# Kernel tuning notes

Measured on AMD Instinct MI355X. Metric: run time of the kernel, lower is better.

The kernel has to match this reference:

```python
import jax, jax.numpy as jnp
import numpy as np

EPS = 1e-7  # K.epsilon()
ROUTINGS = 3
NUM_CAPSULE = 32
DIM_CAPSULE = 16


def squash(x, axis=-1):
    s = jnp.sum(jnp.square(x), axis=axis, keepdims=True) + EPS
    scale = jnp.sqrt(s) / (0.5 + s)
    return scale * x


def setup_inputs() -> dict:
    key = jax.random.key(0)
    k1, k2 = jax.random.split(key)
    inputs = jax.random.normal(k1, (128, 1024, 128), dtype=jnp.float32)
    kernel = jax.random.normal(k2, (1, 128, NUM_CAPSULE * DIM_CAPSULE), dtype=jnp.float32) * 0.05
    return {"inputs": inputs, "kernel": kernel}


def reference(inputs, kernel):
    B, In, D = inputs.shape
    # shared-weight conv1d with kernel size 1 == GEMM over last dim
    hat = jnp.einsum('bid,dk->bik', inputs, kernel[0])  # (B, In, N*dc)
    hat = hat.reshape(B, In, NUM_CAPSULE, DIM_CAPSULE).transpose(0, 2, 1, 3)  # (B, N, In, dc)
    b = jnp.zeros((B, NUM_CAPSULE, In), dtype=hat.dtype)
    o = None
    for i in range(ROUTINGS):
        c = jax.nn.softmax(b, axis=1)                     # softmax over num_capsule
        o = squash(jnp.einsum('bni,bnid->bnd', c, hat))   # (B, N, dc)
        if i < ROUTINGS - 1:
            b = jnp.einsum('bnd,bnid->bni', o, hat)       # b = <o, hat> (replace, per code)
    return o
```

## Files before the change

### kernel.cpp

```cpp
#include <hip/hip_runtime.h>

#define BATCH 128
#define SEQ   1024
#define DIM   128
#define NCAP  32
#define DCAPS 16
#define KTOT  512
#define EPS_  1e-7f
#define RCH   8
#define RROWS 128

#define OFF_SPART 0
#define OFF_WT    (OFF_SPART + BATCH*RCH*DIM)
#define OFF_UBF   (OFF_WT + KTOT*DIM)
#define OFF_VP    (OFF_UBF + BATCH*NCAP*DIM/2)
#define OFF_XROW  (OFF_VP + BATCH*RCH*NCAP*DIM)
#define OFF_XT    (OFF_XROW + BATCH*SEQ*DIM/2)

typedef __attribute__((ext_vector_type(8))) short short8v;
typedef __attribute__((ext_vector_type(4))) float f32x4;
typedef unsigned short ushort_t;

__device__ __forceinline__ unsigned f2bf(float f) {
  unsigned u = __float_as_uint(f);
  u += 0x7fffu + ((u >> 16) & 1u);
  return u >> 16;
}
__device__ __forceinline__ uint4 pack8(float4 a, float4 b) {
  uint4 r;
  r.x = f2bf(a.x) | (f2bf(a.y) << 16);
  r.y = f2bf(a.z) | (f2bf(a.w) << 16);
  r.z = f2bf(b.x) | (f2bf(b.y) << 16);
  r.w = f2bf(b.z) | (f2bf(b.w) << 16);
  return r;
}

__global__ __launch_bounds__(256)
void k_pre(const float* __restrict__ x, const float* __restrict__ w,
           float* __restrict__ ws) {
  int t = threadIdx.x;
  __shared__ __align__(16) char smem[40960];

  if (blockIdx.y == BATCH) {
    float* wl = (float*)smem;
    int k0 = blockIdx.x * 64;
    for (int it = 0; it < 32; ++it) {
      int f = it * 256 + t;
      int kk = f & 63, d = f >> 6;
      wl[d * 66 + kk] = w[d * KTOT + k0 + kk];
    }
    __syncthreads();
    float* wt = ws + OFF_WT;
    for (int it = 0; it < 32; ++it) {
      int f = it * 256 + t;
      int d = f & 127, kk = f >> 7;
      wt[(size_t)(k0 + kk) * DIM + d] = wl[d * 66 + kk];
    }
    return;
  }
  int b = blockIdx.y, ch = blockIdx.x;
  ushort_t* xl = (ushort_t*)smem;
  float4* red0 = (float4*)(smem + 32768);
  float4* red1 = (float4*)(smem + 32768 + 4096);

  const float4* X4 = (const float4*)(x + ((size_t)b * SEQ + (size_t)ch * RROWS) * DIM);
  ushort_t* xrow = (ushort_t*)(ws + OFF_XROW) + ((size_t)b * SEQ + (size_t)ch * RROWS) * DIM;
  ushort_t* xt   = (ushort_t*)(ws + OFF_XT)   + (size_t)b * DIM * SEQ;

  int seg = t & 15, grp = t >> 4;
  float4 a0 = make_float4(0.f,0.f,0.f,0.f), a1 = make_float4(0.f,0.f,0.f,0.f);
  for (int it = 0; it < 8; ++it) {
    int r = it * 16 + grp;
    float4 v0 = X4[(size_t)r * 32 + seg * 2];
    float4 v1 = X4[(size_t)r * 32 + seg * 2 + 1];
    a0.x += v0.x; a0.y += v0.y; a0.z += v0.z; a0.w += v0.w;
    a1.x += v1.x; a1.y += v1.y; a1.z += v1.z; a1.w += v1.w;
    uint4 pk = pack8(v0, v1);
    *(uint4*)(xrow + (size_t)r * DIM + seg * 8) = pk;
    *(uint4*)(smem + r * 256 + ((seg << 4) ^ (((r >> 3) & 7) << 4))) = pk;
  }
  red0[grp * 16 + seg] = a0;
  red1[grp * 16 + seg] = a1;
  __syncthreads();

  if (t < 128) {
    int sg = t >> 3, e = t & 7;
    float s = 0.f;
    for (int g = 0; g < 16; ++g) {
      const float* p0 = (const float*)&red0[g * 16 + sg];
      const float* p1 = (const float*)&red1[g * 16 + sg];
      s += (e < 4) ? p0[e] : p1[e - 4];
    }
    ws[OFF_SPART + ((size_t)b * RCH + ch) * DIM + t] = s;
  }

  for (int j = 0; j < 8; ++j) {
    int f = j * 256 + t;
    int r8g = f & 15;
    int d   = f >> 4;
    int dhi = (d >> 3) << 4, dlo = (d & 7) * 2;
    int rsw = (r8g & 7) << 4;
    const char* base = smem + ((dhi ^ rsw) + dlo);
    union { ushort_t s[8]; uint4 v; } tmp;
    #pragma unroll
    for (int i = 0; i < 8; ++i)
      tmp.s[i] = *(const ushort_t*)(base + (r8g * 8 + i) * 256);
    *(uint4*)(xt + (size_t)d * SEQ + ch * RROWS + r8g * 8) = tmp.v;
  }
}

template<int MODE>
__global__ __launch_bounds__(128)
void k_ou(float* __restrict__ ws, float* __restrict__ outp) {
  int b = blockIdx.y, bx = blockIdx.x, t = threadIdx.x;
  int k = bx * 128 + t;
  __shared__ float vin[8 * DIM];
  __shared__ float osh[128];

  if (MODE == 0) {
    const float* sp = ws + OFF_SPART + (size_t)b * RCH * DIM;
    float s = 0.f;
    for (int c = 0; c < RCH; ++c) s += sp[c * DIM + t];
    vin[t] = s * (1.0f / 32.0f);
  } else {
    const float* vp = ws + OFF_VP + (size_t)b * RCH * NCAP * DIM + (size_t)bx * 8 * DIM;
    for (int j = 0; j < 8; ++j) {
      float s = 0.f;
      for (int c = 0; c < RCH; ++c)
        s += vp[(size_t)c * NCAP * DIM + j * DIM + t];
      vin[j * DIM + t] = s;
    }
  }
  __syncthreads();

  int nl = t >> 4;
  const float4* vr = (const float4*)((MODE == 0) ? vin : (vin + nl * DIM));
  const float4* wtr = (const float4*)(ws + OFF_WT + (size_t)k * DIM);
  float p = 0.f;
  #pragma unroll 8
  for (int i = 0; i < 32; ++i) {
    float4 wv = wtr[i], vv = vr[i];
    p += wv.x * vv.x + wv.y * vv.y + wv.z * vv.z + wv.w * vv.w;
  }

  float sq = p * p;
  sq += __shfl_xor(sq, 1, 16);
  sq += __shfl_xor(sq, 2, 16);
  sq += __shfl_xor(sq, 4, 16);
  sq += __shfl_xor(sq, 8, 16);
  sq += EPS_;
  float scale = sqrtf(sq) / (0.5f + sq);
  float o = scale * p;

  if (MODE == 2) { outp[(size_t)b * KTOT + k] = o; return; }

  osh[t] = o;
  __syncthreads();

  const float* wt = ws + OFF_WT;
  ushort_t* ubf = (ushort_t*)(ws + OFF_UBF) + (size_t)b * NCAP * DIM;
  for (int j = 0; j < 8; ++j) {
    int n = bx * 8 + j;
    float a = 0.f;
    #pragma unroll
    for (int dc = 0; dc < DCAPS; ++dc)
      a += wt[(size_t)(n * DCAPS + dc) * DIM + t] * osh[j * DCAPS + dc];
    ubf[(size_t)n * DIM + t] = (ushort_t)f2bf(a);
  }
}

__global__ __launch_bounds__(256)
void k_route(const float* __restrict__ ws_c, float* __restrict__ vp) {
  __shared__ __align__(16) ushort_t ct_s[NCAP * RROWS];

  int b = blockIdx.y, ch = blockIdx.x, t = threadIdx.x;
  int wv = t >> 6;
  int l  = t & 63;
  int q  = l >> 4;
  int lr = l & 15;

  const ushort_t* ubf  = (const ushort_t*)(ws_c + OFF_UBF) + (size_t)b * NCAP * DIM;
  const ushort_t* xrow = (const ushort_t*)(ws_c + OFF_XROW) + ((size_t)b * SEQ + (size_t)ch * RROWS) * DIM;
  const ushort_t* xt   = (const ushort_t*)(ws_c + OFF_XT)   + (size_t)b * DIM * SEQ + (size_t)ch * RROWS;

  short8v ufr[2][4], xfr[2][4];
  #pragma unroll
  for (int nt = 0; nt < 2; ++nt)
    #pragma unroll
    for (int kk = 0; kk < 4; ++kk)
      ufr[nt][kk] = *(const short8v*)(ubf + (size_t)(nt * 16 + lr) * DIM + kk * 32 + q * 8);
  #pragma unroll
  for (int rt = 0; rt < 2; ++rt)
    #pragma unroll
    for (int kk = 0; kk < 4; ++kk)
      xfr[rt][kk] = *(const short8v*)(xrow + (size_t)(wv * 32 + rt * 16 + lr) * DIM + kk * 32 + q * 8);

  f32x4 acc[2][2];
  #pragma unroll
  for (int rt = 0; rt < 2; ++rt)
    #pragma unroll
    for (int nt = 0; nt < 2; ++nt)
      acc[rt][nt] = (f32x4){0.f, 0.f, 0.f, 0.f};

  #pragma unroll
  for (int kk = 0; kk < 4; ++kk)
    #pragma unroll
    for (int rt = 0; rt < 2; ++rt)
      #pragma unroll
      for (int nt = 0; nt < 2; ++nt)
        acc[rt][nt] = __builtin_amdgcn_mfma_f32_16x16x32_bf16(
            ufr[nt][kk], xfr[rt][kk], acc[rt][nt], 0, 0, 0);

  short8v axfr[2][4];
  #pragma unroll
  for (int dt = 0; dt < 2; ++dt)
    #pragma unroll
    for (int kk = 0; kk < 4; ++kk)
      axfr[dt][kk] = *(const short8v*)(xt + (size_t)(wv * 32 + dt * 16 + lr) * SEQ + kk * 32 + q * 8);

  #pragma unroll
  for (int rt = 0; rt < 2; ++rt) {
    float v[8];
    #pragma unroll
    for (int nt = 0; nt < 2; ++nt)
      #pragma unroll
      for (int j = 0; j < 4; ++j) v[nt * 4 + j] = acc[rt][nt][j];
    float m = v[0];
    #pragma unroll
    for (int i = 1; i < 8; ++i) m = fmaxf(m, v[i]);
    m = fmaxf(m, __shfl_xor(m, 16));
    m = fmaxf(m, __shfl_xor(m, 32));
    float e[8], s = 0.f;
    #pragma unroll
    for (int i = 0; i < 8; ++i) { e[i] = __expf(v[i] - m); s += e[i]; }
    s += __shfl_xor(s, 16);
    s += __shfl_xor(s, 32);
    float inv = 1.0f / s;
    int r = wv * 32 + rt * 16 + lr;
    int rs = r >> 3, rb = (r & 7) * 2;
    #pragma unroll
    for (int nt = 0; nt < 2; ++nt)
      #pragma unroll
      for (int j = 0; j < 4; ++j) {
        int n = nt * 16 + q * 4 + j;
        *(ushort_t*)((char*)ct_s + n * 256 + ((rs ^ (n & 15)) << 4) + rb) =
            (ushort_t)f2bf(e[nt * 4 + j] * inv);
      }
  }

  __syncthreads();

  short8v bc[2][4];
  #pragma unroll
  for (int nt = 0; nt < 2; ++nt) {
    int n2 = nt * 16 + lr;
    #pragma unroll
    for (int kk = 0; kk < 4; ++kk)
      bc[nt][kk] = *(const short8v*)((char*)ct_s + n2 * 256 + (((4 * kk + q) ^ (n2 & 15)) << 4));
  }

  f32x4 vac[2][2];
  #pragma unroll
  for (int dt = 0; dt < 2; ++dt)
    #pragma unroll
    for (int nt = 0; nt < 2; ++nt)
      vac[dt][nt] = (f32x4){0.f, 0.f, 0.f, 0.f};

  #pragma unroll
  for (int kk = 0; kk < 4; ++kk)
    #pragma unroll
    for (int dt = 0; dt < 2; ++dt)
      #pragma unroll
      for (int nt = 0; nt < 2; ++nt)
        vac[dt][nt] = __builtin_amdgcn_mfma_f32_16x16x32_bf16(
            axfr[dt][kk], bc[nt][kk], vac[dt][nt], 0, 0, 0);

  float* vo = vp + ((size_t)(b * RCH + ch) * NCAP) * DIM;
  #pragma unroll
  for (int dt = 0; dt < 2; ++dt)
    #pragma unroll
    for (int nt = 0; nt < 2; ++nt) {
      int n = nt * 16 + lr;
      int d0 = wv * 32 + dt * 16 + q * 4;
      *(f32x4*)(vo + (size_t)n * DIM + d0) = vac[dt][nt];
    }
}

extern "C" void kernel_launch(void* const* d_in, const int* in_sizes, int n_in,
                              void* d_out, int out_size, void* d_ws, size_t ws_size,
                              hipStream_t stream) {
  (void)in_sizes; (void)n_in; (void)out_size; (void)ws_size;
  const float* x = (const float*)d_in[0];
  const float* w = (const float*)d_in[1];
  float* out = (float*)d_out;
  float* ws  = (float*)d_ws;
  float* wsvp = ws + OFF_VP;

  k_pre<<<dim3(8, BATCH + 1), 256, 0, stream>>>(x, w, ws);
  k_ou<0><<<dim3(4, BATCH), 128, 0, stream>>>(ws, out);
  k_route<<<dim3(RCH, BATCH), 256, 0, stream>>>(ws, wsvp);
  k_ou<1><<<dim3(4, BATCH), 128, 0, stream>>>(ws, out);
  k_route<<<dim3(RCH, BATCH), 256, 0, stream>>>(ws, wsvp);
  k_ou<2><<<dim3(4, BATCH), 128, 0, stream>>>(ws, out);
}
```

Baseline: 84.97 us.

## Drop global transposed x copy; stage x tile in LDS for both MFMA operands

The pre-pass no longer writes a transposed bf16 copy of the inputs to global memory. Instead the routing kernel loads its 128x128 bf16 x tile into a padded LDS layout once and reads it both row-wise and column-wise for the two MFMA GEMMs. This removes a full global write and re-read of the transposed tensor, plus the LDS transpose work in k_pre. The cost is more LDS use per block in k_route, an extra barrier, and scalar 2-byte LDS gathers to build the transposed operand, which may limit occupancy or cause bank conflicts.

```diff
diff --git a/kernel.cpp b/kernel.cpp
--- a/kernel.cpp
+++ b/kernel.cpp
@@ -15,11 +15,14 @@
 #define OFF_UBF   (OFF_WT + KTOT*DIM)
 #define OFF_VP    (OFF_UBF + BATCH*NCAP*DIM/2)
 #define OFF_XROW  (OFF_VP + BATCH*RCH*NCAP*DIM)
-#define OFF_XT    (OFF_XROW + BATCH*SEQ*DIM/2)
 
 typedef __attribute__((ext_vector_type(8))) short short8v;
 typedef __attribute__((ext_vector_type(4))) float f32x4;
 typedef unsigned short ushort_t;
+
+#define SUBOFF(r4, d16) (((r4)*8 + (d16))*176)
+#define CTOFF 45056
+#define SMEMSZ (CTOFF + 8192)
 
 __device__ __forceinline__ unsigned f2bf(float f) {
   unsigned u = __float_as_uint(f);
@@ -39,7 +42,7 @@
 void k_pre(const float* __restrict__ x, const float* __restrict__ w,
            float* __restrict__ ws) {
   int t = threadIdx.x;
-  __shared__ __align__(16) char smem[40960];
+  __shared__ __align__(16) char smem[33792];
 
   if (blockIdx.y == BATCH) {
     float* wl = (float*)smem;
@@ -59,13 +62,11 @@
     return;
   }
   int b = blockIdx.y, ch = blockIdx.x;
-  ushort_t* xl = (ushort_t*)smem;
-  float4* red0 = (float4*)(smem + 32768);
-  float4* red1 = (float4*)(smem + 32768 + 4096);
+  float4* red0 = (float4*)smem;
+  float4* red1 = (float4*)(smem + 4096);
 
   const float4* X4 = (const float4*)(x + ((size_t)b * SEQ + (size_t)ch * RROWS) * DIM);
   ushort_t* xrow = (ushort_t*)(ws + OFF_XROW) + ((size_t)b * SEQ + (size_t)ch * RROWS) * DIM;
-  ushort_t* xt   = (ushort_t*)(ws + OFF_XT)   + (size_t)b * DIM * SEQ;
 
   int seg = t & 15, grp = t >> 4;
   float4 a0 = make_float4(0.f,0.f,0.f,0.f), a1 = make_float4(0.f,0.f,0.f,0.f);
@@ -75,9 +76,7 @@
     float4 v1 = X4[(size_t)r * 32 + seg * 2 + 1];
     a0.x += v0.x; a0.y += v0.y; a0.z += v0.z; a0.w += v0.w;
     a1.x += v1.x; a1.y += v1.y; a1.z += v1.z; a1.w += v1.w;
-    uint4 pk = pack8(v0, v1);
-    *(uint4*)(xrow + (size_t)r * DIM + seg * 8) = pk;
-    *(uint4*)(smem + r * 256 + ((seg << 4) ^ (((r >> 3) & 7) << 4))) = pk;
+    *(uint4*)(xrow + (size_t)r * DIM + seg * 8) = pack8(v0, v1);
   }
   red0[grp * 16 + seg] = a0;
   red1[grp * 16 + seg] = a1;
@@ -92,20 +91,6 @@
       s += (e < 4) ? p0[e] : p1[e - 4];
     }
     ws[OFF_SPART + ((size_t)b * RCH + ch) * DIM + t] = s;
-  }
-
-  for (int j = 0; j < 8; ++j) {
-    int f = j * 256 + t;
-    int r8g = f & 15;
-    int d   = f >> 4;
-    int dhi = (d >> 3) << 4, dlo = (d & 7) * 2;
-    int rsw = (r8g & 7) << 4;
-    const char* base = smem + ((dhi ^ rsw) + dlo);
-    union { ushort_t s[8]; uint4 v; } tmp;
-    #pragma unroll
-    for (int i = 0; i < 8; ++i)
-      tmp.s[i] = *(const ushort_t*)(base + (r8g * 8 + i) * 256);
-    *(uint4*)(xt + (size_t)d * SEQ + ch * RROWS + r8g * 8) = tmp.v;
   }
 }
 
@@ -171,7 +156,7 @@
 
 __global__ __launch_bounds__(256)
 void k_route(const float* __restrict__ ws_c, float* __restrict__ vp) {
-  __shared__ __align__(16) ushort_t ct_s[NCAP * RROWS];
+  __shared__ __align__(16) char smem[SMEMSZ];
 
   int b = blockIdx.y, ch = blockIdx.x, t = threadIdx.x;
   int wv = t >> 6;
@@ -181,19 +166,23 @@
 
   const ushort_t* ubf  = (const ushort_t*)(ws_c + OFF_UBF) + (size_t)b * NCAP * DIM;
   const ushort_t* xrow = (const ushort_t*)(ws_c + OFF_XROW) + ((size_t)b * SEQ + (size_t)ch * RROWS) * DIM;
-  const ushort_t* xt   = (const ushort_t*)(ws_c + OFF_XT)   + (size_t)b * DIM * SEQ + (size_t)ch * RROWS;
-
-  short8v ufr[2][4], xfr[2][4];
+
+  #pragma unroll
+  for (int it = 0; it < 8; ++it) {
+    int f = it * 256 + t;
+    int r = f >> 4, d0 = (f & 15) * 8;
+    uint4 v = *(const uint4*)(xrow + (size_t)r * DIM + d0);
+    *(uint4*)(smem + SUBOFF(r >> 2, d0 >> 4) + (r & 3) * 32 + ((d0 & 15) << 1)) = v;
+  }
+
+  short8v ufr[2][4];
   #pragma unroll
   for (int nt = 0; nt < 2; ++nt)
     #pragma unroll
     for (int kk = 0; kk < 4; ++kk)
       ufr[nt][kk] = *(const short8v*)(ubf + (size_t)(nt * 16 + lr) * DIM + kk * 32 + q * 8);
-  #pragma unroll
-  for (int rt = 0; rt < 2; ++rt)
-    #pragma unroll
-    for (int kk = 0; kk < 4; ++kk)
-      xfr[rt][kk] = *(const short8v*)(xrow + (size_t)(wv * 32 + rt * 16 + lr) * DIM + kk * 32 + q * 8);
+
+  __syncthreads();
 
   f32x4 acc[2][2];
   #pragma unroll
@@ -203,20 +192,18 @@
       acc[rt][nt] = (f32x4){0.f, 0.f, 0.f, 0.f};
 
   #pragma unroll
-  for (int kk = 0; kk < 4; ++kk)
-    #pragma unroll
-    for (int rt = 0; rt < 2; ++rt)
+  for (int kk = 0; kk < 4; ++kk) {
+    #pragma unroll
+    for (int rt = 0; rt < 2; ++rt) {
+      int r = wv * 32 + rt * 16 + lr;
+      short8v xf = *(const short8v*)(smem + SUBOFF(r >> 2, 2 * kk + (q >> 1))
+                                     + (r & 3) * 32 + (q & 1) * 16);
       #pragma unroll
       for (int nt = 0; nt < 2; ++nt)
         acc[rt][nt] = __builtin_amdgcn_mfma_f32_16x16x32_bf16(
-            ufr[nt][kk], xfr[rt][kk], acc[rt][nt], 0, 0, 0);
-
-  short8v axfr[2][4];
-  #pragma unroll
-  for (int dt = 0; dt < 2; ++dt)
-    #pragma unroll
-    for (int kk = 0; kk < 4; ++kk)
-      axfr[dt][kk] = *(const short8v*)(xt + (size_t)(wv * 32 + dt * 16 + lr) * SEQ + kk * 32 + q * 8);
+            ufr[nt][kk], xf, acc[rt][nt], 0, 0, 0);
+    }
+  }
 
   #pragma unroll
   for (int rt = 0; rt < 2; ++rt) {
@@ -243,7 +230,7 @@
       #pragma unroll
       for (int j = 0; j < 4; ++j) {
         int n = nt * 16 + q * 4 + j;
-        *(ushort_t*)((char*)ct_s + n * 256 + ((rs ^ (n & 15)) << 4) + rb) =
+        *(ushort_t*)(smem + CTOFF + n * 256 + ((rs ^ (n & 15)) << 4) + rb) =
             (ushort_t)f2bf(e[nt * 4 + j] * inv);
       }
   }
@@ -256,7 +243,7 @@
     int n2 = nt * 16 + lr;
     #pragma unroll
     for (int kk = 0; kk < 4; ++kk)
-      bc[nt][kk] = *(const short8v*)((char*)ct_s + n2 * 256 + (((4 * kk + q) ^ (n2 & 15)) << 4));
+      bc[nt][kk] = *(const short8v*)(smem + CTOFF + n2 * 256 + (((4 * kk + q) ^ (n2 & 15)) << 4));
   }
 
   f32x4 vac[2][2];
@@ -267,13 +254,21 @@
       vac[dt][nt] = (f32x4){0.f, 0.f, 0.f, 0.f};
 
   #pragma unroll
-  for (int kk = 0; kk < 4; ++kk)
-    #pragma unroll
-    for (int dt = 0; dt < 2; ++dt)
-      #pragma unroll
-      for (int nt = 0; nt < 2; ++nt)
-        vac[dt][nt] = __builtin_amdgcn_mfma_f32_16x16x32_bf16(
-            axfr[dt][kk], bc[nt][kk], vac[dt][nt], 0, 0, 0);
+  for (int kk = 0; kk < 4; ++kk) {
+    union { short8v v; ushort_t s[8]; } ax0, ax1;
+    #pragma unroll
+    for (int e = 0; e < 8; ++e) {
+      int r4 = kk * 8 + q * 2 + (e >> 2);
+      int boff = (e & 3) * 32 + lr * 2;
+      ax0.s[e] = *(const ushort_t*)(smem + SUBOFF(r4, wv * 2    ) + boff);
+      ax1.s[e] = *(const ushort_t*)(smem + SUBOFF(r4, wv * 2 + 1) + boff);
+    }
+    #pragma unroll
+    for (int nt = 0; nt < 2; ++nt) {
+      vac[0][nt] = __builtin_amdgcn_mfma_f32_16x16x32_bf16(ax0.v, bc[nt][kk], vac[0][nt], 0, 0, 0);
+      vac[1][nt] = __builtin_amdgcn_mfma_f32_16x16x32_bf16(ax1.v, bc[nt][kk], vac[1][nt], 0, 0, 0);
+    }
+  }
 
   float* vo = vp + ((size_t)(b * RCH + ch) * NCAP) * DIM;
   #pragma unroll
```

Result: faster. 73.93 us (-13.0%).
